# Optimization experiments

Measured on AMD Instinct MI355X. Metric: run time of the kernel, lower is better.

## Reference

```python
import jax, jax.numpy as jnp
import numpy as np

EPS = 1e-10

def setup_inputs() -> dict:
    key = jax.random.key(0)
    ks = jax.random.split(key, 7)
    B, S, C, H, W = 8, 4, 512, 64, 64
    Cq = C // 4
    x = jax.random.normal(ks[0], (B, S, C, H, W), dtype=jnp.float32)
    wq = jax.random.normal(ks[1], (S, Cq, C), dtype=jnp.float32) * 0.02
    bq = jax.random.normal(ks[2], (S, Cq), dtype=jnp.float32) * 0.02
    wk = jax.random.normal(ks[3], (S, Cq, C), dtype=jnp.float32) * 0.02
    bk = jax.random.normal(ks[4], (S, Cq), dtype=jnp.float32) * 0.02
    wv = jax.random.normal(ks[5], (S, C, C), dtype=jnp.float32) * 0.02
    bv = jax.random.normal(ks[6], (S, C), dtype=jnp.float32) * 0.02
    gamma = jnp.zeros((1,), dtype=jnp.float32)
    return {"x": x, "wq": wq, "bq": bq, "wk": wk, "bk": bk,
            "wv": wv, "bv": bv, "gamma": gamma}

def reference(x, wq, bq, wk, bk, wv, bv, gamma):
    # x: (B, S, C, H, W); per-scale 1x1 convs == per-pixel matmuls
    B, S, C, H, W = x.shape
    q = jnp.einsum('bschw,soc->bsohw', x, wq) + bq[None, :, :, None, None]
    k = jnp.einsum('bschw,soc->bsohw', x, wk) + bk[None, :, :, None, None]
    v = jnp.einsum('bschw,soc->bsohw', x, wv) + bv[None, :, :, None, None]
    pq = q.reshape(B, S, -1)                      # (B, S, D)
    pk = k.reshape(B, S, -1).transpose(0, 2, 1)   # (B, D, S)
    pv = v.reshape(B, S, -1)                      # (B, S, C*H*W)
    # L2 normalization (cosine similarity), matching torch eps placement
    A1 = pq / (jnp.sqrt(jnp.sum(pq * pq, axis=-1, keepdims=True)) + EPS)
    B1 = pk / (jnp.sqrt(jnp.sum(pk * pk, axis=1, keepdims=True)) + EPS)
    energy = jnp.einsum('bsd,bdt->bst', A1, B1)   # (B, S, S)
    attention = jax.nn.softmax(energy, axis=-1)
    out = jnp.einsum('bst,btd->bsd', attention, pv).reshape(B, S, C, H, W)
    out = gamma[0] * out + x
    # original returns list [out[:, i]] for i in range(S); return stacked tensor
    return out
```

## Files before the change

kernel.cpp:

```cpp
#include <hip/hip_runtime.h>
#include <hip/hip_bf16.h>

#define EPS_F 1e-10f

typedef short s16x8 __attribute__((ext_vector_type(8)));
typedef float f32x4 __attribute__((ext_vector_type(4)));
typedef unsigned short ushort_t;

constexpr int B_ = 8, S_ = 4, C_ = 512, Cq_ = 128, HW_ = 4096;
constexpr long long D_ = (long long)Cq_ * HW_;

__device__ inline float bf_lo(unsigned int u) { return __uint_as_float(u << 16); }
__device__ inline float bf_hi(unsigned int u) { return __uint_as_float(u & 0xffff0000u); }

__device__ inline ushort_t f2bf(float f) {
    __hip_bfloat16 h = __float2bfloat16(f);
    return *reinterpret_cast<ushort_t*>(&h);
}
__device__ inline unsigned int pack_bf2(float a, float b) {
    return (unsigned int)f2bf(a) | ((unsigned int)f2bf(b) << 16);
}
__device__ inline float dot8(uint4 a, uint4 b) {
    return bf_lo(a.x) * bf_lo(b.x) + bf_hi(a.x) * bf_hi(b.x)
         + bf_lo(a.y) * bf_lo(b.y) + bf_hi(a.y) * bf_hi(b.y)
         + bf_lo(a.z) * bf_lo(b.z) + bf_hi(a.z) * bf_hi(b.z)
         + bf_lo(a.w) * bf_lo(b.w) + bf_hi(a.w) * bf_hi(b.w);
}

#define GLOAD16(gp, lp) __builtin_amdgcn_global_load_lds( \
    (const __attribute__((address_space(1))) unsigned int*)(gp), \
    (__attribute__((address_space(3))) unsigned int*)(lp), 16, 0, 0)

#define VMCNT0 asm volatile("s_waitcnt vmcnt(0)" ::: "memory")
#define LGK0   asm volatile("s_waitcnt lgkmcnt(0)" ::: "memory")
#define MFMA16(a, b, c) __builtin_amdgcn_mfma_f32_16x16x32_bf16(a, b, c, 0, 0, 0)

#define SWZ(p) ((((p) >> 3) & 7) ^ ((p) & 7))

__global__ __launch_bounds__(256) void prep3(
    const float* __restrict__ wq, const float* __restrict__ wk,
    const float* __restrict__ wv,
    ushort_t* __restrict__ Wqk_pre, ushort_t* __restrict__ Wvb_pre,
    float* __restrict__ g4) {
    int gid = blockIdx.x * 256 + threadIdx.x;
    if (gid < 8 * 24 * 16) g4[gid] = 0.f;
    if (gid < 65536) {
        int s = gid >> 14;
        int kt = (gid >> 11) & 7;
        int row = (gid >> 3) & 255;
        int slot = gid & 7;
        int col = kt * 64 + ((slot ^ (row & 7)) << 3);
        const float* src = (row < 128)
            ? &wq[((size_t)s * 128 + row) * 512 + col]
            : &wk[((size_t)s * 128 + (row - 128)) * 512 + col];
        float4 f0 = *reinterpret_cast<const float4*>(src);
        float4 f1 = *reinterpret_cast<const float4*>(src + 4);
        uint4 o;
        o.x = pack_bf2(f0.x, f0.y); o.y = pack_bf2(f0.z, f0.w);
        o.z = pack_bf2(f1.x, f1.y); o.w = pack_bf2(f1.z, f1.w);
        *reinterpret_cast<uint4*>(Wqk_pre + (size_t)gid * 8) = o;
    } else {
        int c2 = gid - 65536;
        int t = c2 >> 15;
        int ct = (c2 >> 14) & 1;
        int kt = (c2 >> 11) & 7;
        int row = (c2 >> 3) & 255;
        int slot = c2 & 7;
        int col = kt * 64 + ((slot ^ (row & 7)) << 3);
        const float* src = &wv[((size_t)t * 512 + ct * 256 + row) * 512 + col];
        float4 f0 = *reinterpret_cast<const float4*>(src);
        float4 f1 = *reinterpret_cast<const float4*>(src + 4);
        uint4 o;
        o.x = pack_bf2(f0.x, f0.y); o.y = pack_bf2(f0.z, f0.w);
        o.z = pack_bf2(f1.x, f1.y); o.w = pack_bf2(f1.z, f1.w);
        *reinterpret_cast<uint4*>(Wvb_pre + (size_t)c2 * 8) = o;
    }
}

#define DECLS_COMMON_QK()                                                    \
    const int tid = threadIdx.x;                                             \
    const int w = tid >> 6, lane = tid & 63;                                 \
    const int w4 = w * 4;                                                    \
    const int wr = w >> 1, wc = w & 1;                                       \
    const int li = lane & 15, lk = lane >> 4;                                \
    const int arow = wr * 64;                                                \
    const int bp = wc * 16 + li;                                             \
    int a_sl[2], b_sl[2];                                                    \
    _Pragma("unroll")                                                        \
    for (int h = 0; h < 2; ++h) {                                            \
        a_sl[h] = (((h * 4 + lk) ^ (li & 7)) << 3);                          \
        b_sl[h] = (((h * 4 + lk) ^ SWZ(bp)) << 3);                           \
    }

__global__ __launch_bounds__(512, 4) void qk6(
    const ushort_t* __restrict__ Wqk_pre, const float* __restrict__ x,
    const float* __restrict__ bq, const float* __restrict__ bk,
    ushort_t* __restrict__ Qb, ushort_t* __restrict__ Kb,
    ushort_t* __restrict__ xbfT) {

    const int xcd = blockIdx.x & 7;
    const int idx = blockIdx.x >> 3;
    const int bt = xcd * 4 + (idx >> 7);
    const int s = bt & 3;
    const int p0 = (idx & 127) * 32;

    __shared__ __align__(16) ushort_t AsAll[2 * 16384];
    __shared__ __align__(16) ushort_t BsAll[2 * 2048];

    DECLS_COMMON_QK();

    const int sk = tid >> 3, spb = (tid & 7) * 4;
    const int ep = tid >> 3, esl = tid & 7;
    const int ec = esl ^ SWZ(ep);

    const float* Bx = x + (size_t)bt * C_ * HW_ + p0 + spb;

    f32x4 acc[4];
#pragma unroll
    for (int mf = 0; mf < 4; ++mf) acc[mf] = 0.f;

    float4 nb;

#define STAGE_A6(T, BUF)                                                     \
    { const ushort_t* _tp = Wqk_pre + ((size_t)(s * 8 + (T)) << 14);         \
      ushort_t* _ld = &AsAll[(BUF) * 16384];                                 \
      _Pragma("unroll")                                                      \
      for (int _i = 0; _i < 4; ++_i)                                         \
          GLOAD16(_tp + ((w4 + _i) << 9) + (lane << 3),                      \
                  _ld + ((w4 + _i) << 9)); }

#define LOAD_B6(T) nb = *reinterpret_cast<const float4*>(Bx + (size_t)((T) * 64 + sk) * HW_)

#define WRITE_B6(BUF)                                                        \
    { float _vv[4] = {nb.x, nb.y, nb.z, nb.w};                               \
      _Pragma("unroll")                                                      \
      for (int _j = 0; _j < 4; ++_j) {                                       \
          int _p = spb + _j;                                                 \
          BsAll[(BUF) * 2048 + _p * 64 + (((sk >> 3) ^ SWZ(_p)) << 3)        \
                + (sk & 7)] = f2bf(_vv[_j]);                                 \
      } }

#define EMIT6(T, BUF)                                                        \
    if (w < 4) {                                                             \
        s16x8 _ev = *reinterpret_cast<const s16x8*>(&BsAll[(BUF) * 2048 + tid * 8]); \
        *reinterpret_cast<s16x8*>(                                           \
            xbfT + ((size_t)bt * HW_ + p0 + ep) * 512 + (T) * 64 + ec * 8) = _ev; \
    }

#define COMPUTE6Q(BUF)                                                       \
    { const int _ab = (BUF) * 16384, _bb = (BUF) * 2048;                     \
      _Pragma("unroll")                                                      \
      for (int h = 0; h < 2; ++h) {                                          \
          s16x8 af0 = *reinterpret_cast<const s16x8*>(                       \
              &AsAll[_ab + (arow + 0 * 16 + li) * 64 + a_sl[h]]);            \
          s16x8 af1 = *reinterpret_cast<const s16x8*>(                       \
              &AsAll[_ab + (arow + 1 * 16 + li) * 64 + a_sl[h]]);            \
          s16x8 af2 = *reinterpret_cast<const s16x8*>(                       \
              &AsAll[_ab + (arow + 2 * 16 + li) * 64 + a_sl[h]]);            \
          s16x8 af3 = *reinterpret_cast<const s16x8*>(                       \
              &AsAll[_ab + (arow + 3 * 16 + li) * 64 + a_sl[h]]);            \
          s16x8 bf = *reinterpret_cast<const s16x8*>(                        \
              &BsAll[_bb + bp * 64 + b_sl[h]]);                              \
          __builtin_amdgcn_s_setprio(1);                                     \
          acc[0] = MFMA16(af0, bf, acc[0]);                                  \
          acc[1] = MFMA16(af1, bf, acc[1]);                                  \
          acc[2] = MFMA16(af2, bf, acc[2]);                                  \
          acc[3] = MFMA16(af3, bf, acc[3]);                                  \
          __builtin_amdgcn_s_setprio(0);                                     \
      } }

    LOAD_B6(0);
    STAGE_A6(0, 0);
    WRITE_B6(0);
    VMCNT0; LGK0;
    __builtin_amdgcn_s_barrier();

#pragma unroll
    for (int t = 0; t < 8; ++t) {
        if (t < 7) { LOAD_B6(t + 1); STAGE_A6(t + 1, (t + 1) & 1); }
        EMIT6(t, t & 1);
        COMPUTE6Q(t & 1);
        if (t < 7) {
            WRITE_B6((t + 1) & 1);
            VMCNT0; LGK0;
            __builtin_amdgcn_s_barrier();
        }
    }

#undef STAGE_A6
#undef LOAD_B6
#undef WRITE_B6
#undef EMIT6
#undef COMPUTE6Q

#pragma unroll
    for (int mf = 0; mf < 4; ++mf) {
#pragma unroll
        for (int r = 0; r < 4; ++r) {
            int m = wr * 64 + mf * 16 + lk * 4 + r;
            float bias = (m < 128) ? bq[s * 128 + m] : bk[s * 128 + (m - 128)];
            int p = p0 + wc * 16 + li;
            float vv = acc[mf][r] + bias;
            if (m < 128)
                Qb[(size_t)bt * D_ + (size_t)m * HW_ + p] = f2bf(vv);
            else
                Kb[(size_t)bt * D_ + (size_t)(m - 128) * HW_ + p] = f2bf(vv);
        }
    }
}

__global__ __launch_bounds__(256, 4) void vblend7(
    const ushort_t* __restrict__ Wvb_pre, const ushort_t* __restrict__ xbfT,
    const float* __restrict__ x, const float* __restrict__ bv,
    const float* __restrict__ att, const float* __restrict__ gamma,
    float* __restrict__ out) {

    const int b = blockIdx.x & 7;
    const int idx = blockIdx.x >> 3;
    const int cblk = idx >> 6;
    const int p0 = (idx & 63) * 64;
    const int ct = cblk >> 2;
    const int csub = cblk & 3;

    __shared__ __align__(16) ushort_t AsAll[2 * 4096];
    __shared__ __align__(16) ushort_t BsAll[2 * 4096];

    const int tid = threadIdx.x;
    const int w = tid >> 6, lane = tid & 63;
    const int wr2 = w >> 1, wc2 = w & 1;
    const int li = lane & 15, lk = lane >> 4;

    int a_sl[2], b_sl[2];
    const int bp = wc2 * 32 + li;
    const int bp1 = bp + 16;
    int b_sl1[2];
#pragma unroll
    for (int h = 0; h < 2; ++h) {
        a_sl[h] = (((h * 4 + lk) ^ (li & 7)) << 3);
        b_sl[h] = (((h * 4 + lk) ^ SWZ(bp)) << 3);
        b_sl1[h] = (((h * 4 + lk) ^ SWZ(bp1)) << 3);
    }

    float attv[16];
#pragma unroll
    for (int i = 0; i < 16; ++i)
        attv[i] = __uint_as_float(__builtin_amdgcn_readfirstlane(
            __float_as_uint(att[b * 16 + i])));

    const int bst_p0 = tid >> 3, bst_sl0 = tid & 7;
    const int bst_c0 = bst_sl0 ^ SWZ(bst_p0);
    const int bst_p1 = (tid + 256) >> 3, bst_sl1 = tid & 7;
    const int bst_c1 = bst_sl1 ^ SWZ(bst_p1);

    f32x4 acc[2][2];
    f32x4 mst[4][2][2];
#pragma unroll
    for (int mf = 0; mf < 2; ++mf)
#pragma unroll
        for (int nf = 0; nf < 2; ++nf) acc[mf][nf] = 0.f;
#pragma unroll
    for (int so = 0; so < 4; ++so)
#pragma unroll
        for (int mf = 0; mf < 2; ++mf)
#pragma unroll
            for (int nf = 0; nf < 2; ++nf) mst[so][mf][nf] = 0.f;

#define STAGE7(TS, BUF)                                                      \
    {   const int _t = (TS) >> 3, _kt = (TS) & 7;                            \
        const ushort_t* _ap = Wvb_pre +                                      \
            (((size_t)(_t * 2 + ct) * 8 + _kt) << 14) + (csub << 12);        \
        ushort_t* _al = &AsAll[(BUF) * 4096];                                \
        GLOAD16(_ap + (size_t)(w << 9) + (size_t)((lane & 63) << 3),         \
                _al + (w << 9));                                             \
        GLOAD16(_ap + 2048 + (size_t)(w << 9) + (size_t)(lane << 3),         \
                _al + 2048 + (w << 9));                                      \
        const ushort_t* _bb = xbfT + ((size_t)(b * 4 + _t) * HW_);           \
        GLOAD16(_bb + ((size_t)(p0 + bst_p0)) * 512 + _kt * 64 + bst_c0 * 8, \
                &BsAll[(BUF) * 4096 + (w << 9)]);                            \
        GLOAD16(_bb + ((size_t)(p0 + bst_p1)) * 512 + _kt * 64 + bst_c1 * 8, \
                &BsAll[(BUF) * 4096 + 2048 + (w << 9)]);                     \
    }

#define COMPUTE7(BUF)                                                       \
    {   const int _ab = (BUF) * 4096, _bbf = (BUF) * 4096;                  \
        _Pragma("unroll")                                                    \
        for (int h = 0; h < 2; ++h) {                                        \
            s16x8 af0 = *reinterpret_cast<const s16x8*>(                     \
                &AsAll[_ab + (wr2 * 32 + 0 * 16 + li) * 64 + a_sl[h]]);      \
            s16x8 af1 = *reinterpret_cast<const s16x8*>(                     \
                &AsAll[_ab + (wr2 * 32 + 1 * 16 + li) * 64 + a_sl[h]]);      \
            s16x8 bf0 = *reinterpret_cast<const s16x8*>(                     \
                &BsAll[_bbf + bp * 64 + b_sl[h]]);                           \
            s16x8 bf1 = *reinterpret_cast<const s16x8*>(                     \
                &BsAll[_bbf + bp1 * 64 + b_sl1[h]]);                         \
            __builtin_amdgcn_s_setprio(1);                                   \
            acc[0][0] = MFMA16(af0, bf0, acc[0][0]);                         \
            acc[0][1] = MFMA16(af0, bf1, acc[0][1]);                         \
            acc[1][0] = MFMA16(af1, bf0, acc[1][0]);                         \
            acc[1][1] = MFMA16(af1, bf1, acc[1][1]);                         \
            __builtin_amdgcn_s_setprio(0);                                   \
        } }

#define BLEND7(T2)                                                           \
    { _Pragma("unroll")                                                      \
      for (int _so = 0; _so < 4; ++_so)                                      \
          _Pragma("unroll")                                                  \
          for (int _mf = 0; _mf < 2; ++_mf)                                  \
              _Pragma("unroll")                                              \
              for (int _nf = 0; _nf < 2; ++_nf)                              \
                  mst[_so][_mf][_nf] += attv[_so * 4 + (T2)] * acc[_mf][_nf];\
      _Pragma("unroll")                                                      \
      for (int _mf = 0; _mf < 2; ++_mf)                                      \
          _Pragma("unroll")                                                  \
          for (int _nf = 0; _nf < 2; ++_nf) acc[_mf][_nf] = 0.f; }

    STAGE7(0, 0);
    VMCNT0;
    __builtin_amdgcn_s_barrier();

#pragma unroll
    for (int ts = 0; ts < 32; ++ts) {
        if (ts < 31) STAGE7(ts + 1, (ts + 1) & 1);
        COMPUTE7(ts & 1);
        if (ts == 7)  BLEND7(0);
        if (ts == 15) BLEND7(1);
        if (ts == 23) BLEND7(2);
        if (ts == 31) BLEND7(3);
        if (ts < 31) {
            VMCNT0;
            __builtin_amdgcn_s_barrier();
        }
    }

#undef STAGE7
#undef COMPUTE7
#undef BLEND7

    const float gm = gamma[0];
    const int c0 = cblk * 64;
#pragma unroll
    for (int mf = 0; mf < 2; ++mf) {
#pragma unroll
        for (int r = 0; r < 4; ++r) {
            int c = c0 + wr2 * 32 + mf * 16 + lk * 4 + r;
            float bvv[4];
#pragma unroll
            for (int t = 0; t < 4; ++t) bvv[t] = bv[(size_t)t * 512 + c];
#pragma unroll
            for (int so = 0; so < 4; ++so) {
                float bsum = attv[so * 4 + 0] * bvv[0] + attv[so * 4 + 1] * bvv[1]
                           + attv[so * 4 + 2] * bvv[2] + attv[so * 4 + 3] * bvv[3];
#pragma unroll
                for (int nf = 0; nf < 2; ++nf) {
                    int p = p0 + wc2 * 32 + nf * 16 + li;
                    size_t off = ((size_t)(b * 4 + so) * C_ + c) * HW_ + p;
                    out[off] = gm * (mst[so][mf][nf][r] + bsum) + x[off];
                }
            }
        }
    }
}

__global__ __launch_bounds__(256) void gram5(
    const ushort_t* __restrict__ Q, const ushort_t* __restrict__ K,
    float* __restrict__ g4) {

    const int ch = blockIdx.x;
    const int b  = blockIdx.y;
    const size_t base = (size_t)ch * (D_ / 16);

    const uint4* qv[4];
    const uint4* kv[4];
#pragma unroll
    for (int s = 0; s < 4; ++s) {
        qv[s] = reinterpret_cast<const uint4*>(Q + (size_t)(b * 4 + s) * D_ + base);
        kv[s] = reinterpret_cast<const uint4*>(K + (size_t)(b * 4 + s) * D_ + base);
    }

    float accr[24];
#pragma unroll
    for (int e = 0; e < 24; ++e) accr[e] = 0.f;

    const int n8 = (int)(D_ / 16 / 8);
    for (int i = threadIdx.x; i < n8; i += 256) {
        uint4 qa[4], ka[4];
#pragma unroll
        for (int s = 0; s < 4; ++s) { qa[s] = qv[s][i]; ka[s] = kv[s][i]; }
#pragma unroll
        for (int s = 0; s < 4; ++s) {
#pragma unroll
            for (int u = 0; u < 4; ++u) accr[s * 4 + u] += dot8(qa[s], ka[u]);
            accr[16 + s] += dot8(qa[s], qa[s]);
            accr[20 + s] += dot8(ka[s], ka[s]);
        }
    }

    __shared__ float red[4][24];
    const int lane = threadIdx.x & 63, wid = threadIdx.x >> 6;
#pragma unroll
    for (int e = 0; e < 24; ++e) {
        float v = accr[e];
#pragma unroll
        for (int o = 32; o > 0; o >>= 1) v += __shfl_down(v, o);
        if (lane == 0) red[wid][e] = v;
    }
    __syncthreads();
    if (threadIdx.x < 24) {
        float t = red[0][threadIdx.x] + red[1][threadIdx.x]
                + red[2][threadIdx.x] + red[3][threadIdx.x];
        g4[((size_t)b * 24 + threadIdx.x) * 16 + ch] = t;
    }
}

__global__ void att_k5(const float* __restrict__ g4, float* __restrict__ att) {
    const int b = threadIdx.x;
    if (b >= B_) return;
    float e_[24];
#pragma unroll
    for (int e = 0; e < 24; ++e) {
        const float* p = g4 + ((size_t)b * 24 + e) * 16;
        float t = 0.f;
#pragma unroll
        for (int ch = 0; ch < 16; ++ch) t += p[ch];
        e_[e] = t;
    }
    float nq[4], nk[4];
#pragma unroll
    for (int s = 0; s < 4; ++s) {
        nq[s] = sqrtf(e_[16 + s]) + EPS_F;
        nk[s] = sqrtf(e_[20 + s]) + EPS_F;
    }
#pragma unroll
    for (int s = 0; s < 4; ++s) {
        float e[4], m = -1e30f;
#pragma unroll
        for (int t = 0; t < 4; ++t) {
            e[t] = e_[s * 4 + t] / (nq[s] * nk[t]);
            m = fmaxf(m, e[t]);
        }
        float sum = 0.f;
#pragma unroll
        for (int t = 0; t < 4; ++t) { e[t] = expf(e[t] - m); sum += e[t]; }
#pragma unroll
        for (int t = 0; t < 4; ++t) att[(size_t)(b * 4 + s) * 4 + t] = e[t] / sum;
    }
}

extern "C" void kernel_launch(void* const* d_in, const int* in_sizes, int n_in,
                              void* d_out, int out_size, void* d_ws, size_t ws_size,
                              hipStream_t stream) {
    const float* x     = (const float*)d_in[0];
    const float* wq    = (const float*)d_in[1];
    const float* bq    = (const float*)d_in[2];
    const float* wk    = (const float*)d_in[3];
    const float* bk    = (const float*)d_in[4];
    const float* wv    = (const float*)d_in[5];
    const float* bv    = (const float*)d_in[6];
    const float* gamma = (const float*)d_in[7];
    float* out = (float*)d_out;

    char* ws = (char*)d_ws;
    const size_t qk_elems = (size_t)B_ * S_ * Cq_ * HW_;
    ushort_t* Qb      = (ushort_t*)ws;
    ushort_t* Kb      = Qb + qk_elems;
    ushort_t* Wqk_pre = Kb + qk_elems;
    ushort_t* Wvb_pre = Wqk_pre + (size_t)4 * 8 * 256 * 64;
    float*    g4      = (float*)(Wvb_pre + (size_t)4 * 2 * 8 * 256 * 64);
    float*    att     = g4 + 8 * 24 * 16;
    ushort_t* xbfT    = (ushort_t*)(att + 128);

    prep3<<<768, 256, 0, stream>>>(wq, wk, wv, Wqk_pre, Wvb_pre, g4);
    qk6<<<4096, 512, 0, stream>>>(Wqk_pre, x, bq, bk, Qb, Kb, xbfT);
    gram5<<<dim3(16, 8), 256, 0, stream>>>(Qb, Kb, g4);
    att_k5<<<1, 64, 0, stream>>>(g4, att);
    vblend7<<<4096, 256, 0, stream>>>(Wvb_pre, xbfT, x, bv, att, gamma, out);
}
```

Measured before the change: 429.7 us.

## Split QK projection blocks by Q/K half and reorder vblend block mapping

The QK projection kernel now launches twice as many blocks, each computing only the Q or only the K half (128 output channels). This halves per-block LDS and accumulators and raises the occupancy hint. The cost is that each x tile is loaded and converted to bf16 twice, though only the Q half writes the transposed bf16 copy. Separately, the vblend kernel's block index now puts the channel block in the fast-varying bits, so neighbouring blocks share the same pixel tile, which is meant to improve cache reuse of xbfT and x.

```diff
diff --git a/kernel.cpp b/kernel.cpp
--- a/kernel.cpp
+++ b/kernel.cpp
@@ -77,22 +77,7 @@
     }
 }
 
-#define DECLS_COMMON_QK()                                                    \
-    const int tid = threadIdx.x;                                             \
-    const int w = tid >> 6, lane = tid & 63;                                 \
-    const int w4 = w * 4;                                                    \
-    const int wr = w >> 1, wc = w & 1;                                       \
-    const int li = lane & 15, lk = lane >> 4;                                \
-    const int arow = wr * 64;                                                \
-    const int bp = wc * 16 + li;                                             \
-    int a_sl[2], b_sl[2];                                                    \
-    _Pragma("unroll")                                                        \
-    for (int h = 0; h < 2; ++h) {                                            \
-        a_sl[h] = (((h * 4 + lk) ^ (li & 7)) << 3);                          \
-        b_sl[h] = (((h * 4 + lk) ^ SWZ(bp)) << 3);                           \
-    }
-
-__global__ __launch_bounds__(512, 4) void qk6(
+__global__ __launch_bounds__(512, 8) void qk8(
     const ushort_t* __restrict__ Wqk_pre, const float* __restrict__ x,
     const float* __restrict__ bq, const float* __restrict__ bk,
     ushort_t* __restrict__ Qb, ushort_t* __restrict__ Kb,
@@ -100,14 +85,27 @@
 
     const int xcd = blockIdx.x & 7;
     const int idx = blockIdx.x >> 3;
-    const int bt = xcd * 4 + (idx >> 7);
+    const int bt = xcd * 4 + (idx >> 8);
     const int s = bt & 3;
-    const int p0 = (idx & 127) * 32;
-
-    __shared__ __align__(16) ushort_t AsAll[2 * 16384];
+    const int pb = (idx >> 1) & 127;
+    const int ob = idx & 1;
+    const int p0 = pb * 32;
+
+    __shared__ __align__(16) ushort_t AsAll[2 * 8192];
     __shared__ __align__(16) ushort_t BsAll[2 * 2048];
 
-    DECLS_COMMON_QK();
+    const int tid = threadIdx.x;
+    const int w = tid >> 6, lane = tid & 63;
+    const int wr = w >> 1, wc = w & 1;
+    const int li = lane & 15, lk = lane >> 4;
+    const int arow = wr * 32;
+    const int bp = wc * 16 + li;
+    int a_sl[2], b_sl[2];
+#pragma unroll
+    for (int h = 0; h < 2; ++h) {
+        a_sl[h] = (((h * 4 + lk) ^ (li & 7)) << 3);
+        b_sl[h] = (((h * 4 + lk) ^ SWZ(bp)) << 3);
+    }
 
     const int sk = tid >> 3, spb = (tid & 7) * 4;
     const int ep = tid >> 3, esl = tid & 7;
@@ -115,23 +113,22 @@
 
     const float* Bx = x + (size_t)bt * C_ * HW_ + p0 + spb;
 
-    f32x4 acc[4];
-#pragma unroll
-    for (int mf = 0; mf < 4; ++mf) acc[mf] = 0.f;
-
+    f32x4 acc[2];
+    acc[0] = 0.f; acc[1] = 0.f;
     float4 nb;
 
-#define STAGE_A6(T, BUF)                                                     \
-    { const ushort_t* _tp = Wqk_pre + ((size_t)(s * 8 + (T)) << 14);         \
-      ushort_t* _ld = &AsAll[(BUF) * 16384];                                 \
+#define STAGE_A8(T, BUF)                                                     \
+    { const ushort_t* _tp = Wqk_pre + ((size_t)(s * 8 + (T)) << 14)          \
+                            + (ob << 13);                                    \
+      ushort_t* _ld = &AsAll[(BUF) * 8192];                                  \
       _Pragma("unroll")                                                      \
-      for (int _i = 0; _i < 4; ++_i)                                         \
-          GLOAD16(_tp + ((w4 + _i) << 9) + (lane << 3),                      \
-                  _ld + ((w4 + _i) << 9)); }
-
-#define LOAD_B6(T) nb = *reinterpret_cast<const float4*>(Bx + (size_t)((T) * 64 + sk) * HW_)
-
-#define WRITE_B6(BUF)                                                        \
+      for (int _i = 0; _i < 2; ++_i)                                         \
+          GLOAD16(_tp + ((w * 2 + _i) << 9) + (lane << 3),                   \
+                  _ld + ((w * 2 + _i) << 9)); }
+
+#define LOAD_B8(T) nb = *reinterpret_cast<const float4*>(Bx + (size_t)((T) * 64 + sk) * HW_)
+
+#define WRITE_B8(BUF)                                                        \
     { float _vv[4] = {nb.x, nb.y, nb.z, nb.w};                               \
       _Pragma("unroll")                                                      \
       for (int _j = 0; _j < 4; ++_j) {                                       \
@@ -140,76 +137,68 @@
                 + (sk & 7)] = f2bf(_vv[_j]);                                 \
       } }
 
-#define EMIT6(T, BUF)                                                        \
-    if (w < 4) {                                                             \
+#define EMIT8(T, BUF)                                                        \
+    if (ob == 0 && w < 4) {                                                  \
         s16x8 _ev = *reinterpret_cast<const s16x8*>(&BsAll[(BUF) * 2048 + tid * 8]); \
         *reinterpret_cast<s16x8*>(                                           \
             xbfT + ((size_t)bt * HW_ + p0 + ep) * 512 + (T) * 64 + ec * 8) = _ev; \
     }
 
-#define COMPUTE6Q(BUF)                                                       \
-    { const int _ab = (BUF) * 16384, _bb = (BUF) * 2048;                     \
+#define COMPUTE8(BUF)                                                        \
+    { const int _ab = (BUF) * 8192, _bb = (BUF) * 2048;                      \
       _Pragma("unroll")                                                      \
       for (int h = 0; h < 2; ++h) {                                          \
           s16x8 af0 = *reinterpret_cast<const s16x8*>(                       \
               &AsAll[_ab + (arow + 0 * 16 + li) * 64 + a_sl[h]]);            \
           s16x8 af1 = *reinterpret_cast<const s16x8*>(                       \
               &AsAll[_ab + (arow + 1 * 16 + li) * 64 + a_sl[h]]);            \
-          s16x8 af2 = *reinterpret_cast<const s16x8*>(                       \
-              &AsAll[_ab + (arow + 2 * 16 + li) * 64 + a_sl[h]]);            \
-          s16x8 af3 = *reinterpret_cast<const s16x8*>(                       \
-              &AsAll[_ab + (arow + 3 * 16 + li) * 64 + a_sl[h]]);            \
           s16x8 bf = *reinterpret_cast<const s16x8*>(                        \
               &BsAll[_bb + bp * 64 + b_sl[h]]);                              \
           __builtin_amdgcn_s_setprio(1);                                     \
           acc[0] = MFMA16(af0, bf, acc[0]);                                  \
           acc[1] = MFMA16(af1, bf, acc[1]);                                  \
-          acc[2] = MFMA16(af2, bf, acc[2]);                                  \
-          acc[3] = MFMA16(af3, bf, acc[3]);                                  \
           __builtin_amdgcn_s_setprio(0);                                     \
       } }
 
-    LOAD_B6(0);
-    STAGE_A6(0, 0);
-    WRITE_B6(0);
+    LOAD_B8(0);
+    STAGE_A8(0, 0);
+    WRITE_B8(0);
     VMCNT0; LGK0;
     __builtin_amdgcn_s_barrier();
 
 #pragma unroll
     for (int t = 0; t < 8; ++t) {
-        if (t < 7) { LOAD_B6(t + 1); STAGE_A6(t + 1, (t + 1) & 1); }
-        EMIT6(t, t & 1);
-        COMPUTE6Q(t & 1);
+        if (t < 7) { LOAD_B8(t + 1); STAGE_A8(t + 1, (t + 1) & 1); }
+        EMIT8(t, t & 1);
+        COMPUTE8(t & 1);
         if (t < 7) {
-            WRITE_B6((t + 1) & 1);
+            WRITE_B8((t + 1) & 1);
             VMCNT0; LGK0;
             __builtin_amdgcn_s_barrier();
         }
     }
 
-#undef STAGE_A6
-#undef LOAD_B6
-#undef WRITE_B6
-#undef EMIT6
-#undef COMPUTE6Q
-
-#pragma unroll
-    for (int mf = 0; mf < 4; ++mf) {
+#undef STAGE_A8
+#undef LOAD_B8
+#undef WRITE_B8
+#undef EMIT8
+#undef COMPUTE8
+
+    ushort_t* outp = ob ? Kb : Qb;
+    const float* biasp = ob ? (bk + s * 128) : (bq + s * 128);
+#pragma unroll
+    for (int mf = 0; mf < 2; ++mf) {
 #pragma unroll
         for (int r = 0; r < 4; ++r) {
-            int m = wr * 64 + mf * 16 + lk * 4 + r;
-            float bias = (m < 128) ? bq[s * 128 + m] : bk[s * 128 + (m - 128)];
+            int m = arow + mf * 16 + lk * 4 + r;
+            float vv = acc[mf][r] + biasp[m];
             int p = p0 + wc * 16 + li;
-            float vv = acc[mf][r] + bias;
-            if (m < 128)
-                Qb[(size_t)bt * D_ + (size_t)m * HW_ + p] = f2bf(vv);
-            else
-                Kb[(size_t)bt * D_ + (size_t)(m - 128) * HW_ + p] = f2bf(vv);
-        }
-    }
-}
-
-__global__ __launch_bounds__(256, 4) void vblend7(
+            outp[(size_t)bt * D_ + (size_t)m * HW_ + p] = f2bf(vv);
+        }
+    }
+}
+
+__global__ __launch_bounds__(256, 4) void vblend8(
     const ushort_t* __restrict__ Wvb_pre, const ushort_t* __restrict__ xbfT,
     const float* __restrict__ x, const float* __restrict__ bv,
     const float* __restrict__ att, const float* __restrict__ gamma,
@@ -217,8 +206,8 @@
 
     const int b = blockIdx.x & 7;
     const int idx = blockIdx.x >> 3;
-    const int cblk = idx >> 6;
-    const int p0 = (idx & 63) * 64;
+    const int cblk = idx & 7;
+    const int p0 = (idx >> 3) * 64;
     const int ct = cblk >> 2;
     const int csub = cblk & 3;
 
@@ -270,7 +259,7 @@
         const ushort_t* _ap = Wvb_pre +                                      \
             (((size_t)(_t * 2 + ct) * 8 + _kt) << 14) + (csub << 12);        \
         ushort_t* _al = &AsAll[(BUF) * 4096];                                \
-        GLOAD16(_ap + (size_t)(w << 9) + (size_t)((lane & 63) << 3),         \
+        GLOAD16(_ap + (size_t)(w << 9) + (size_t)(lane << 3),                \
                 _al + (w << 9));                                             \
         GLOAD16(_ap + 2048 + (size_t)(w << 9) + (size_t)(lane << 3),         \
                 _al + 2048 + (w << 9));                                      \
@@ -470,8 +459,8 @@
     ushort_t* xbfT    = (ushort_t*)(att + 128);
 
     prep3<<<768, 256, 0, stream>>>(wq, wk, wv, Wqk_pre, Wvb_pre, g4);
-    qk6<<<4096, 512, 0, stream>>>(Wqk_pre, x, bq, bk, Qb, Kb, xbfT);
+    qk8<<<8192, 512, 0, stream>>>(Wqk_pre, x, bq, bk, Qb, Kb, xbfT);
     gram5<<<dim3(16, 8), 256, 0, stream>>>(Qb, Kb, g4);
     att_k5<<<1, 64, 0, stream>>>(g4, att);
-    vblend7<<<4096, 256, 0, stream>>>(Wvb_pre, xbfT, x, bv, att, gamma, out);
-}
+    vblend8<<<4096, 256, 0, stream>>>(Wvb_pre, xbfT, x, bv, att, gamma, out);
+}
```

Measured after the change: 405.6 us. 1.06x faster.
